# Kernel optimization log

Measured on AMD Instinct MI355X. Metric: run time of the kernel, lower is better.

Reference implementation:

```python
import jax, jax.numpy as jnp
import numpy as np
import math

def _ln(x, g, b, eps=1e-5):
    mu = x.mean(-1, keepdims=True)
    var = ((x - mu) ** 2).mean(-1, keepdims=True)
    return (x - mu) / jnp.sqrt(var + eps) * g + b

def _mha(x, in_w, in_b, out_w, out_b, nh):
    # torch nn.MultiheadAttention (batch_first, eval): q,k,v chunks of in_proj
    Bn, Nn, Dm = x.shape
    hd = Dm // nh
    q, k, v = jnp.split(x @ in_w.T + in_b, 3, axis=-1)
    sp = lambda t: t.reshape(Bn, Nn, nh, hd).transpose(0, 2, 1, 3)
    q, k, v = sp(q), sp(k), sp(v)
    a = jax.nn.softmax(jnp.einsum('bhid,bhjd->bhij', q, k) / math.sqrt(hd), axis=-1)
    y = jnp.einsum('bhij,bhjd->bhid', a, v).transpose(0, 2, 1, 3).reshape(Bn, Nn, Dm)
    return y @ out_w.T + out_b

def setup_inputs():
    key = jax.random.key(0)
    ks = iter(jax.random.split(key, 40))
    nrm = lambda shape: jax.random.normal(next(ks), shape, jnp.float32) * 0.02
    B, T, C, H, W = 2, 32, 3, 64, 64
    D, P, nL, nS = 512, 8, 6, 3
    N = (H // P) ** 2
    z = lambda *s: jnp.zeros(s, jnp.float32)
    o = lambda *s: jnp.ones(s, jnp.float32)
    return dict(
        x=jax.random.normal(next(ks), (B, T, C, H, W), jnp.float32),
        patch_w=nrm((D, C * P * P)), patch_b=z(D),
        tok_ln_g=o(D), tok_ln_b=z(D),
        spatial_pos=nrm((1, 1, N, D)), temporal_pos=nrm((1, T, 1, D)),
        snorm_g=o(D), snorm_b=z(D),
        sa_in_w=nrm((nS, 3 * D, D)), sa_in_b=z(nS, 3 * D),
        sa_out_w=nrm((nS, D, D)), sa_out_b=z(nS, D),
        ln1_g=o(nL, D), ln1_b=z(nL, D),
        kqv_w=nrm((nL, 3 * D, D)), kqv_b=z(nL, 3 * D),
        proj_w=nrm((nL, D, D)), proj_b=z(nL, D),
        ln2_g=o(nL, D), ln2_b=z(nL, D),
        fc_w=nrm((nL, 4 * D, D)), fc_b=z(nL, 4 * D),
        cproj_w=nrm((nL, D, 4 * D)), cproj_b=z(nL, D),
        lnf_g=o(D), lnf_b=z(D),
        th_w1=nrm((D // 2, D)), th_b1=z(D // 2), th_w2=nrm((1, D // 2)), th_b2=z(1),
        sh_w1=nrm((D // 2, D)), sh_b1=z(D // 2), sh_w2=nrm((1, D // 2)), sh_b2=z(1),
        pf_w1=nrm((D // 2, D)), pf_b1=z(D // 2), pf_w2=nrm((1, D // 2)), pf_b2=z(1),
    )

def reference(x, patch_w, patch_b, tok_ln_g, tok_ln_b, spatial_pos, temporal_pos,
              snorm_g, snorm_b, sa_in_w, sa_in_b, sa_out_w, sa_out_b,
              ln1_g, ln1_b, kqv_w, kqv_b, proj_w, proj_b, ln2_g, ln2_b,
              fc_w, fc_b, cproj_w, cproj_b, lnf_g, lnf_b,
              th_w1, th_b1, th_w2, th_b2, sh_w1, sh_b1, sh_w2, sh_b2,
              pf_w1, pf_b1, pf_w2, pf_b2):
    B, T, C, H, W = x.shape
    D = patch_w.shape[0]
    P = int(math.isqrt(patch_w.shape[1] // C))
    Hn, Wn = H // P, W // P
    N = Hn * Wn
    # Conv3d kernel=(1,P,P), stride=(1,P,P) == per-frame patchify + matmul
    patches = x.reshape(B, T, C, Hn, P, Wn, P).transpose(0, 1, 3, 5, 2, 4, 6).reshape(B, T, N, C * P * P)
    tok = _ln(patches @ patch_w.T + patch_b, tok_ln_g, tok_ln_b)
    tok = tok + spatial_pos + temporal_pos[:, :T]
    # per-frame spatial attention: identical math per frame -> batch over B*T
    s = tok.reshape(B * T, N, D)
    for i in range(sa_in_w.shape[0]):
        s = s + _mha(_ln(s, snorm_g, snorm_b), sa_in_w[i], sa_in_b[i], sa_out_w[i], sa_out_b[i], nh=4)
    L = T * N
    hid = s.reshape(B, L, D)
    nh = 8
    hd = D // nh
    mask = jnp.tril(jnp.ones((L, L), bool))  # causal over T*N tokens
    for i in range(kqv_w.shape[0]):
        a_in = _ln(hid, ln1_g[i], ln1_b[i])
        k, q, v = jnp.split(a_in @ kqv_w[i].T + kqv_b[i], 3, axis=-1)  # torch split order: k, q, v
        sp = lambda t: t.reshape(B, L, nh, hd).transpose(0, 2, 1, 3)
        q, k, v = sp(q), sp(k), sp(v)
        att = jnp.einsum('bhid,bhjd->bhij', q, k) / math.sqrt(hd)
        att = jax.nn.softmax(jnp.where(mask, att, -jnp.inf), axis=-1)
        y = jnp.einsum('bhij,bhjd->bhid', att, v).transpose(0, 2, 1, 3).reshape(B, L, D)
        hid = hid + y @ proj_w[i].T + proj_b[i]
        m_in = _ln(hid, ln2_g[i], ln2_b[i])
        h = jax.nn.gelu(m_in @ fc_w[i].T + fc_b[i], approximate=False)
        hid = hid + h @ cproj_w[i].T + cproj_b[i]
    hid = _ln(hid, lnf_g, lnf_b).reshape(B, T, N, D)
    head = lambda zz, w1, b1, w2, b2: jax.nn.leaky_relu(zz @ w1.T + b1, 0.2) @ w2.T + b2
    tf = hid.mean(axis=2)  # [B, T, D]
    temporal_score = head(tf[:, -1], th_w1, th_b1, th_w2, th_b2)  # [B, 1] (last timestep, full lengths)
    spatial_score = head(hid.mean(axis=1).mean(axis=1), sh_w1, sh_b1, sh_w2, sh_b2)
    per_frame_scores = head(tf, pf_w1, pf_b1, pf_w2, pf_b2)  # [B, T, 1]
    final_score = temporal_score + spatial_score + per_frame_scores.mean(axis=1)
    return (temporal_score, spatial_score, per_frame_scores, final_score)
```

## Files before the change

kernel.cpp:

```cpp
#include <hip/hip_runtime.h>
#include <hip/hip_bf16.h>
#include <math.h>

#define MTOK 4096

typedef __bf16 bf16x8 __attribute__((ext_vector_type(8)));
typedef float f32x4 __attribute__((ext_vector_type(4)));

__device__ __forceinline__ ushort f2bf(float f){
  __hip_bfloat16 h = __float2bfloat16(f);
  return *reinterpret_cast<ushort*>(&h);
}
__device__ __forceinline__ float bf2f(ushort u){
  return __uint_as_float(((uint)u) << 16);
}
__device__ __forceinline__ void gload_lds16(const void* g, void* l){
  __builtin_amdgcn_global_load_lds((__attribute__((address_space(1))) void*)(void*)g,
                                   (__attribute__((address_space(3))) void*)l, 16, 0, 0);
}

__device__ __forceinline__ float blockReduceSum(float v, float* red){
  #pragma unroll
  for (int off = 32; off; off >>= 1) v += __shfl_down(v, off, 64);
  int lane = threadIdx.x & 63, wid = threadIdx.x >> 6;
  __syncthreads();
  if (lane == 0) red[wid] = v;
  __syncthreads();
  float r = 0.f;
  int nw = blockDim.x >> 6;
  for (int i = 0; i < nw; i++) r += red[i];
  return r;
}
__device__ __forceinline__ float rowMax16(float v){
  #pragma unroll
  for (int m = 8; m; m >>= 1) v = fmaxf(v, __shfl_xor(v, m, 64));
  return v;
}
__device__ __forceinline__ float rowSum16(float v){
  #pragma unroll
  for (int m = 8; m; m >>= 1) v += __shfl_xor(v, m, 64);
  return v;
}

__global__ __launch_bounds__(256) void cvt_w_kernel(
    const float* __restrict__ src, ushort* __restrict__ dst, int n)
{
  int i = (blockIdx.x * 256 + threadIdx.x) * 8;
  float4 a = *(const float4*)(src + i);
  float4 b = *(const float4*)(src + i + 4);
  uint4 o;
  o.x = (uint)f2bf(a.x) | ((uint)f2bf(a.y) << 16);
  o.y = (uint)f2bf(a.z) | ((uint)f2bf(a.w) << 16);
  o.z = (uint)f2bf(b.x) | ((uint)f2bf(b.y) << 16);
  o.w = (uint)f2bf(b.z) | ((uint)f2bf(b.w) << 16);
  *(uint4*)(dst + i) = o;
}

#define OFF_PATCH 0u
#define OFF_SAIN  98304u
#define OFF_SAOUT 2457600u
#define OFF_KQV   3244032u
#define OFF_PROJ  7962624u
#define OFF_FC    9535488u
#define OFF_CPROJ 15826944u
#define W_TOTAL   22118400u
__global__ __launch_bounds__(256) void cvt_all_kernel(
    const float* __restrict__ pw, const float* __restrict__ sain,
    const float* __restrict__ saout, const float* __restrict__ kqv,
    const float* __restrict__ proj, const float* __restrict__ fc,
    const float* __restrict__ cproj, ushort* __restrict__ dst)
{
  int blk = blockIdx.x;
  const float* src; size_t off;
  if      (blk <    48){ src = pw;    off = OFF_PATCH; }
  else if (blk <  1200){ src = sain;  off = OFF_SAIN;  blk -= 48;   }
  else if (blk <  1584){ src = saout; off = OFF_SAOUT; blk -= 1200; }
  else if (blk <  3888){ src = kqv;   off = OFF_KQV;   blk -= 1584; }
  else if (blk <  4656){ src = proj;  off = OFF_PROJ;  blk -= 3888; }
  else if (blk <  7728){ src = fc;    off = OFF_FC;    blk -= 4656; }
  else                 { src = cproj; off = OFF_CPROJ; blk -= 7728; }
  size_t si = (size_t)blk*2048 + threadIdx.x*8;
  float4 a = *(const float4*)(src + si);
  float4 b = *(const float4*)(src + si + 4);
  uint4 o;
  o.x = (uint)f2bf(a.x) | ((uint)f2bf(a.y) << 16);
  o.y = (uint)f2bf(a.z) | ((uint)f2bf(a.w) << 16);
  o.z = (uint)f2bf(b.x) | ((uint)f2bf(b.y) << 16);
  o.w = (uint)f2bf(b.z) | ((uint)f2bf(b.w) << 16);
  *(uint4*)(dst + off + si) = o;
}

__global__ __launch_bounds__(256) void im2col_kernel(
    const float* __restrict__ x, ushort* __restrict__ Pm)
{
  int idx = blockIdx.x*256 + threadIdx.x;
  int m = idx / 24, e8 = idx % 24;
  int b = m >> 11, t = (m >> 6) & 31, n = m & 63;
  int hn = n >> 3, wn = n & 7;
  int c = e8 >> 3, ph = e8 & 7;
  const float* src = x + (((size_t)(b*32 + t)*3 + c)*64 + hn*8 + ph)*64 + wn*8;
  float4 a = *(const float4*)src;
  float4 bq = *(const float4*)(src + 4);
  uint4 o;
  o.x = (uint)f2bf(a.x) | ((uint)f2bf(a.y) << 16);
  o.y = (uint)f2bf(a.z) | ((uint)f2bf(a.w) << 16);
  o.z = (uint)f2bf(bq.x) | ((uint)f2bf(bq.y) << 16);
  o.w = (uint)f2bf(bq.z) | ((uint)f2bf(bq.w) << 16);
  *(uint4*)(Pm + (size_t)m*192 + e8*8) = o;
}

__global__ __launch_bounds__(256) void ln_pos_kernel(
    const float* __restrict__ in, float* __restrict__ out,
    const float* __restrict__ g, const float* __restrict__ b,
    const float* __restrict__ spos, const float* __restrict__ tpos)
{
  int r = blockIdx.x*4 + (threadIdx.x >> 6);
  int lane = threadIdx.x & 63;
  int n = r & 63, t = (r >> 6) & 31;
  const float* row = in + (size_t)r*512 + lane*8;
  float4 v0 = *(const float4*)row;
  float4 v1 = *(const float4*)(row + 4);
  float s = v0.x+v0.y+v0.z+v0.w+v1.x+v1.y+v1.z+v1.w;
  float q = v0.x*v0.x+v0.y*v0.y+v0.z*v0.z+v0.w*v0.w+v1.x*v1.x+v1.y*v1.y+v1.z*v1.z+v1.w*v1.w;
  #pragma unroll
  for (int m = 1; m < 64; m <<= 1){ s += __shfl_xor(s, m, 64); q += __shfl_xor(q, m, 64); }
  float mu = s*(1.f/512.f);
  float inv = rsqrtf(q*(1.f/512.f) - mu*mu + 1e-5f);
  const float* gp = g + lane*8;
  const float* bp = b + lane*8;
  const float* sp = spos + n*512 + lane*8;
  const float* tp = tpos + t*512 + lane*8;
  float* op = out + (size_t)r*512 + lane*8;
  #pragma unroll
  for (int e = 0; e < 2; e++){
    float4 vv = e ? v1 : v0;
    float4 gg = *(const float4*)(gp + e*4);
    float4 bb = *(const float4*)(bp + e*4);
    float4 ss = *(const float4*)(sp + e*4);
    float4 tt = *(const float4*)(tp + e*4);
    float4 oo;
    oo.x = (vv.x-mu)*inv*gg.x + bb.x + ss.x + tt.x;
    oo.y = (vv.y-mu)*inv*gg.y + bb.y + ss.y + tt.y;
    oo.z = (vv.z-mu)*inv*gg.z + bb.z + ss.z + tt.z;
    oo.w = (vv.w-mu)*inv*gg.w + bb.w + ss.w + tt.w;
    *(float4*)(op + e*4) = oo;
  }
}

__global__ __launch_bounds__(256) void ln_bf16_kernel(
    const float* __restrict__ in, ushort* __restrict__ out,
    const float* __restrict__ g, const float* __restrict__ b)
{
  int r = blockIdx.x*4 + (threadIdx.x >> 6);
  int lane = threadIdx.x & 63;
  const float* row = in + (size_t)r*512 + lane*8;
  float4 v0 = *(const float4*)row;
  float4 v1 = *(const float4*)(row + 4);
  float s = v0.x+v0.y+v0.z+v0.w+v1.x+v1.y+v1.z+v1.w;
  float q = v0.x*v0.x+v0.y*v0.y+v0.z*v0.z+v0.w*v0.w+v1.x*v1.x+v1.y*v1.y+v1.z*v1.z+v1.w*v1.w;
  #pragma unroll
  for (int m = 1; m < 64; m <<= 1){ s += __shfl_xor(s, m, 64); q += __shfl_xor(q, m, 64); }
  float mu = s*(1.f/512.f);
  float inv = rsqrtf(q*(1.f/512.f) - mu*mu + 1e-5f);
  float4 g0 = *(const float4*)(g + lane*8);
  float4 g1 = *(const float4*)(g + lane*8 + 4);
  float4 b0 = *(const float4*)(b + lane*8);
  float4 b1 = *(const float4*)(b + lane*8 + 4);
  uint4 o;
  o.x = (uint)f2bf((v0.x-mu)*inv*g0.x + b0.x) | ((uint)f2bf((v0.y-mu)*inv*g0.y + b0.y) << 16);
  o.y = (uint)f2bf((v0.z-mu)*inv*g0.z + b0.z) | ((uint)f2bf((v0.w-mu)*inv*g0.w + b0.w) << 16);
  o.z = (uint)f2bf((v1.x-mu)*inv*g1.x + b1.x) | ((uint)f2bf((v1.y-mu)*inv*g1.y + b1.y) << 16);
  o.w = (uint)f2bf((v1.z-mu)*inv*g1.z + b1.z) | ((uint)f2bf((v1.w-mu)*inv*g1.w + b1.w) << 16);
  *(uint4*)(out + (size_t)r*512 + lane*8) = o;
}

template<int BM, int BN, bool GELU, bool BF16OUT>
__global__ __launch_bounds__(256) void gemm2_kernel(
    const ushort* __restrict__ X, const ushort* __restrict__ Wb,
    const float* __restrict__ bias, const float* __restrict__ res,
    void* __restrict__ Yv, int M, int Nn, int K)
{
  constexpr int WROWS = (BN == 128) ? 2 : 4;
  constexpr int WM = BM / WROWS;
  constexpr int FM = WM / 16;
  constexpr int FN = 4;
  __shared__ __attribute__((aligned(16))) char smem[2*(BM+BN)*128];
  char* Xs0 = smem;
  char* Ws0 = smem + BM*128;
  char* Xs1 = smem + (BM+BN)*128;
  char* Ws1 = Xs1 + BM*128;
  int tid = threadIdx.x, lane = tid & 63, wv = tid >> 6;
  int bm = blockIdx.y * BM, bn = blockIdx.x * BN;
  int wm, wn;
  if (BN == 128){ wm = (wv >> 1) * WM; wn = (wv & 1) * 64; }
  else          { wm = wv * WM;        wn = 0; }

  f32x4 acc[FM][FN];
  #pragma unroll
  for (int i = 0; i < FM; i++)
    #pragma unroll
    for (int j = 0; j < FN; j++){ f32x4 z = {0.f,0.f,0.f,0.f}; acc[i][j] = z; }

  int rowoff = wv*8 + (lane >> 3);
  int colsrc = ((lane & 7) ^ (lane >> 3)) * 16;

  auto stage = [&](char* Xd, char* Wd, int k0){
    #pragma unroll
    for (int i = 0; i < BM/32; i++){
      int row = i*32 + rowoff;
      gload_lds16((const char*)(X + (size_t)(bm + row)*K + k0) + colsrc,
                  Xd + (i*32 + wv*8)*128);
    }
    #pragma unroll
    for (int i = 0; i < BN/32; i++){
      int row = i*32 + rowoff;
      gload_lds16((const char*)(Wb + (size_t)(bn + row)*K + k0) + colsrc,
                  Wd + (i*32 + wv*8)*128);
    }
  };

  stage(Xs0, Ws0, 0);
  __syncthreads();
  int nt = K >> 6;
  for (int t = 0; t < nt; t++){
    char* Xc = (t & 1) ? Xs1 : Xs0;
    char* Wc = (t & 1) ? Ws1 : Ws0;
    if (t + 1 < nt) stage((t & 1) ? Xs0 : Xs1, (t & 1) ? Ws0 : Ws1, (t+1)*64);
    #pragma unroll
    for (int kc = 0; kc < 2; kc++){
      bf16x8 a[FM], b[FN];
      #pragma unroll
      for (int f = 0; f < FM; f++){
        int ra = wm + f*16 + (lane & 15);
        a[f] = *(const bf16x8*)(Xc + ra*128 + ((kc*64 + (lane>>4)*16) ^ ((ra & 7) << 4)));
      }
      #pragma unroll
      for (int f = 0; f < FN; f++){
        int rb = wn + f*16 + (lane & 15);
        b[f] = *(const bf16x8*)(Wc + rb*128 + ((kc*64 + (lane>>4)*16) ^ ((rb & 7) << 4)));
      }
      #pragma unroll
      for (int i = 0; i < FM; i++)
        #pragma unroll
        for (int j = 0; j < FN; j++)
          acc[i][j] = __builtin_amdgcn_mfma_f32_16x16x32_bf16(a[i], b[j], acc[i][j], 0, 0, 0);
    }
    __syncthreads();
  }
  int col0 = lane & 15;
  float bv[FN];
  #pragma unroll
  for (int fn = 0; fn < FN; fn++) bv[fn] = bias[bn + wn + fn*16 + col0];
  #pragma unroll
  for (int fm = 0; fm < FM; fm++){
    #pragma unroll
    for (int r = 0; r < 4; r++){
      int m = bm + wm + fm*16 + (lane >> 4)*4 + r;
      #pragma unroll
      for (int fn = 0; fn < FN; fn++){
        int n = bn + wn + fn*16 + col0;
        float v = acc[fm][fn][r] + bv[fn];
        if (res) v += res[(size_t)m*Nn + n];
        if (GELU) v = 0.5f * v * (1.f + erff(v * 0.70710678118654752440f));
        if (BF16OUT) ((ushort*)Yv)[(size_t)m*Nn + n] = f2bf(v);
        else         ((float*) Yv)[(size_t)m*Nn + n] = v;
      }
    }
  }
}

__global__ __launch_bounds__(256) void spatial_attn_mfma_kernel(
    const ushort* __restrict__ qkv, ushort* __restrict__ y)
{
  __shared__ __attribute__((aligned(16))) char Ks[64*256];
  __shared__ __attribute__((aligned(16))) char Vt[128*128];
  __shared__ __attribute__((aligned(16))) char Ps[64*128];
  int bt = blockIdx.x, h = blockIdx.y;
  int tid = threadIdx.x, lane = tid & 63, w = tid >> 6;
  const ushort* base = qkv + (size_t)bt*64*1536 + (size_t)h*128;
  const float scale = 0.08838834764831845f;

  int qrow = w*16 + (lane & 15);
  bf16x8 qa[4];
  #pragma unroll
  for (int kc = 0; kc < 4; kc++)
    qa[kc] = *(const bf16x8*)(base + (size_t)qrow*1536 + kc*32 + (lane>>4)*8);

  #pragma unroll
  for (int i = 0; i < 4; i++){
    int row = w*16 + i*4 + (lane >> 4);
    const char* src = (const char*)(base + (size_t)row*1536 + 512) + (((lane & 15) ^ (row & 15)) * 16);
    char* dst = Ks + (w*16 + i*4)*256;
    gload_lds16(src, dst);
  }
  {
    int vj = (tid & 31) * 2;
    int d0 = (tid >> 5) * 16;
    const ushort* v0p = base + (size_t)vj*1536 + 1024 + d0;
    const ushort* v1p = v0p + 1536;
    uint4 a0 = *(const uint4*)(v0p);
    uint4 a1 = *(const uint4*)(v0p + 8);
    uint4 b0 = *(const uint4*)(v1p);
    uint4 b1 = *(const uint4*)(v1p + 8);
    uint av[8] = {a0.x, a0.y, a0.z, a0.w, a1.x, a1.y, a1.z, a1.w};
    uint bv[8] = {b0.x, b0.y, b0.z, b0.w, b1.x, b1.y, b1.z, b1.w};
    int cb = 4 * (tid & 31);
    #pragma unroll
    for (int e = 0; e < 8; e++){
      int dl = d0 + e*2, dh = dl + 1;
      uint vlo = (av[e] & 0xffffu) | ((bv[e] & 0xffffu) << 16);
      uint vhi = (av[e] >> 16) | (bv[e] & 0xffff0000u);
      *(uint*)(Vt + dl*128 + (cb ^ ((dl & 7) << 4))) = vlo;
      *(uint*)(Vt + dh*128 + (cb ^ ((dh & 7) << 4))) = vhi;
    }
  }
  __syncthreads();

  f32x4 zero4 = {0.f,0.f,0.f,0.f};
  f32x4 accS[4];
  __builtin_amdgcn_s_setprio(1);
  #pragma unroll
  for (int jt = 0; jt < 4; jt++){
    accS[jt] = zero4;
    #pragma unroll
    for (int kc = 0; kc < 4; kc++){
      int krow = jt*16 + (lane & 15);
      bf16x8 kb = *(const bf16x8*)(Ks + krow*256 + ((kc*64 + (lane>>4)*16) ^ ((krow & 15) << 4)));
      accS[jt] = __builtin_amdgcn_mfma_f32_16x16x32_bf16(qa[kc], kb, accS[jt], 0, 0, 0);
    }
  }
  __builtin_amdgcn_s_setprio(0);
  float l_sum[4];
  #pragma unroll
  for (int r = 0; r < 4; r++){
    float mx = fmaxf(fmaxf(accS[0][r], accS[1][r]), fmaxf(accS[2][r], accS[3][r]));
    mx = rowMax16(mx);
    int prow = w*16 + (lane>>4)*4 + r;
    int swz = (prow & 7) << 4;
    char* pbase = Ps + prow*128;
    float ps = 0.f;
    #pragma unroll
    for (int jt = 0; jt < 4; jt++){
      float p = __expf((accS[jt][r] - mx) * scale);
      ushort pb = f2bf(p);
      *(ushort*)(pbase + ((2*(jt*16 + (lane & 15))) ^ swz)) = pb;
      ps += bf2f(pb);
    }
    l_sum[r] = rowSum16(ps);
  }
  bf16x8 pa[2];
  #pragma unroll
  for (int kc2 = 0; kc2 < 2; kc2++){
    int prow = w*16 + (lane & 15);
    pa[kc2] = *(const bf16x8*)(Ps + prow*128 + ((kc2*64 + (lane>>4)*16) ^ ((prow & 7) << 4)));
  }
  f32x4 o[8];
  __builtin_amdgcn_s_setprio(1);
  #pragma unroll
  for (int dt = 0; dt < 8; dt++){
    o[dt] = zero4;
    #pragma unroll
    for (int kc2 = 0; kc2 < 2; kc2++){
      int vrow = dt*16 + (lane & 15);
      bf16x8 vb = *(const bf16x8*)(Vt + vrow*128 + ((kc2*64 + (lane>>4)*16) ^ ((vrow & 7) << 4)));
      o[dt] = __builtin_amdgcn_mfma_f32_16x16x32_bf16(pa[kc2], vb, o[dt], 0, 0, 0);
    }
  }
  __builtin_amdgcn_s_setprio(0);
  #pragma unroll
  for (int r = 0; r < 4; r++){
    float invl = 1.f / l_sum[r];
    int token = bt*64 + w*16 + (lane>>4)*4 + r;
    ushort* yrow = y + (size_t)token*512 + h*128;
    #pragma unroll
    for (int dt = 0; dt < 8; dt++)
      yrow[dt*16 + (lane & 15)] = f2bf(o[dt][r] * invl);
  }
}

__global__ __launch_bounds__(256) void temporal_attn_split_kernel(
    const ushort* __restrict__ qkv, ushort* __restrict__ Op, float* __restrict__ ml)
{
  __shared__ __attribute__((aligned(16))) char Ks[64*128];
  __shared__ __attribute__((aligned(16))) char Vt[64*128];
  __shared__ __attribute__((aligned(16))) char Ps[4*16*128];
  int id = blockIdx.x;
  int bh = id & 15;
  int rest = id >> 4;
  int qt = 31 - (rest >> 1);
  int half = rest & 1;
  int b = bh >> 3, h = bh & 7;
  int tid = threadIdx.x, lane = tid & 63, w = tid >> 6;
  int g = lane >> 4, q = lane & 15;
  const ushort* base = qkv + (size_t)(b*2048)*1536 + h*64;

  int nk = qt + 1;
  int ktm = (nk + 1) >> 1;
  int kt0 = half ? ktm : 0;
  int kt1 = half ? nk : ktm;

  int qrow = qt*64 + w*16 + q;
  bf16x8 qb[2];
  #pragma unroll
  for (int kc = 0; kc < 2; kc++)
    qb[kc] = *(const bf16x8*)(base + (size_t)qrow*1536 + 512 + kc*32 + g*8);

  f32x4 zero4 = {0.f,0.f,0.f,0.f};
  f32x4 o[4];
  #pragma unroll
  for (int dt = 0; dt < 4; dt++) o[dt] = zero4;
  float m_old = -1e30f, l_sum = 0.f;

  int kcolsrc = ((lane & 7) ^ (lane >> 3)) * 16;
  int vj  = (tid & 31) * 2;
  int vd0 = (tid >> 5) * 8;
  int vcb = 4 * (tid & 31);
  char* myP = Ps + w*2048;
  int pswz = (q & 7) << 4;

  for (int kt = kt0; kt < kt1; kt++){
    __syncthreads();
    #pragma unroll
    for (int i = 0; i < 2; i++){
      int row = w*16 + i*8 + (lane >> 3);
      gload_lds16((const char*)(base + (size_t)(kt*64 + row)*1536) + kcolsrc,
                  Ks + (w*16 + i*8)*128);
    }
    {
      const ushort* v0p = base + (size_t)(kt*64 + vj)*1536 + 1024 + vd0;
      const ushort* v1p = v0p + 1536;
      uint4 a0 = *(const uint4*)v0p;
      uint4 b0 = *(const uint4*)v1p;
      uint av[4] = {a0.x, a0.y, a0.z, a0.w};
      uint bv[4] = {b0.x, b0.y, b0.z, b0.w};
      #pragma unroll
      for (int e = 0; e < 4; e++){
        int dl = vd0 + e*2, dh = dl + 1;
        uint vlo = (av[e] & 0xffffu) | ((bv[e] & 0xffffu) << 16);
        uint vhi = (av[e] >> 16) | (bv[e] & 0xffff0000u);
        *(uint*)(Vt + dl*128 + (vcb ^ ((dl & 7) << 4))) = vlo;
        *(uint*)(Vt + dh*128 + (vcb ^ ((dh & 7) << 4))) = vhi;
      }
    }
    __syncthreads();

    f32x4 accS[4];
    __builtin_amdgcn_s_setprio(1);
    #pragma unroll
    for (int jt = 0; jt < 4; jt++){
      accS[jt] = zero4;
      #pragma unroll
      for (int kc = 0; kc < 2; kc++){
        int krow = jt*16 + q;
        bf16x8 kb = *(const bf16x8*)(Ks + krow*128 + ((kc*64 + g*16) ^ ((krow & 7) << 4)));
        accS[jt] = __builtin_amdgcn_mfma_f32_16x16x32_bf16(kb, qb[kc], accS[jt], 0, 0, 0);
      }
    }
    __builtin_amdgcn_s_setprio(0);
    if (kt == qt){
      int gi = qt*64 + w*16 + q;
      #pragma unroll
      for (int jt = 0; jt < 4; jt++)
        #pragma unroll
        for (int r = 0; r < 4; r++){
          int gj = kt*64 + jt*16 + g*4 + r;
          if (gj > gi) accS[jt][r] = -1e30f;
        }
    }
    float mloc = fmaxf(fmaxf(accS[0][0], accS[0][1]), fmaxf(accS[0][2], accS[0][3]));
    #pragma unroll
    for (int jt = 1; jt < 4; jt++){
      float t2 = fmaxf(fmaxf(accS[jt][0], accS[jt][1]), fmaxf(accS[jt][2], accS[jt][3]));
      mloc = fmaxf(mloc, t2);
    }
    mloc *= 0.125f;
    mloc = fmaxf(mloc, __shfl_xor(mloc, 16, 64));
    mloc = fmaxf(mloc, __shfl_xor(mloc, 32, 64));
    float mnew = fmaxf(m_old, mloc);
    float corr = __expf(m_old - mnew);
    float ps = 0.f;
    #pragma unroll
    for (int jt = 0; jt < 4; jt++){
      ushort pb0 = f2bf(__expf(accS[jt][0]*0.125f - mnew));
      ushort pb1 = f2bf(__expf(accS[jt][1]*0.125f - mnew));
      ushort pb2 = f2bf(__expf(accS[jt][2]*0.125f - mnew));
      ushort pb3 = f2bf(__expf(accS[jt][3]*0.125f - mnew));
      ps += bf2f(pb0) + bf2f(pb1) + bf2f(pb2) + bf2f(pb3);
      uint2 wv;
      wv.x = (uint)pb0 | ((uint)pb1 << 16);
      wv.y = (uint)pb2 | ((uint)pb3 << 16);
      *(uint2*)(myP + q*128 + ((jt*32 + g*8) ^ pswz)) = wv;
    }
    l_sum = l_sum*corr + ps;
    m_old = mnew;
    #pragma unroll
    for (int dt = 0; dt < 4; dt++) o[dt] *= corr;

    bf16x8 pfr[2];
    #pragma unroll
    for (int kc2 = 0; kc2 < 2; kc2++)
      pfr[kc2] = *(const bf16x8*)(myP + q*128 + ((kc2*64 + g*16) ^ pswz));
    __builtin_amdgcn_s_setprio(1);
    #pragma unroll
    for (int dt = 0; dt < 4; dt++){
      #pragma unroll
      for (int kc2 = 0; kc2 < 2; kc2++){
        int vrow = dt*16 + q;
        bf16x8 vb = *(const bf16x8*)(Vt + vrow*128 + ((kc2*64 + g*16) ^ ((vrow & 7) << 4)));
        o[dt] = __builtin_amdgcn_mfma_f32_16x16x32_bf16(vb, pfr[kc2], o[dt], 0, 0, 0);
      }
    }
    __builtin_amdgcn_s_setprio(0);
  }
  l_sum += __shfl_xor(l_sum, 16, 64);
  l_sum += __shfl_xor(l_sum, 32, 64);
  size_t tokbase = (size_t)half*4096 + (size_t)b*2048;
  int token = qt*64 + w*16 + q;
  ushort* yrow = Op + (tokbase + token)*512 + h*64;
  #pragma unroll
  for (int dt = 0; dt < 4; dt++){
    ushort4 o4;
    o4.x = f2bf(o[dt][0]); o4.y = f2bf(o[dt][1]);
    o4.z = f2bf(o[dt][2]); o4.w = f2bf(o[dt][3]);
    *(ushort4*)(yrow + dt*16 + g*4) = o4;
  }
  if (g == 0){
    float* mlp = ml + ((tokbase + token)*8 + h)*2;
    mlp[0] = m_old;
    mlp[1] = l_sum;
  }
}

__global__ __launch_bounds__(256) void attn_merge_kernel(
    const ushort* __restrict__ Op, const float* __restrict__ ml, ushort* __restrict__ Ef)
{
  int tok = blockIdx.x*4 + (threadIdx.x >> 6);
  int l6 = threadIdx.x & 63;
  int h = l6 >> 3, d0 = (l6 & 7)*8;
  int e = h*64 + d0;
  const float* m1p = ml + ((size_t)tok*8 + h)*2;
  const float* m2p = ml + (((size_t)4096 + tok)*8 + h)*2;
  float m1 = m1p[0], l1 = m1p[1];
  float m2 = m2p[0], l2 = m2p[1];
  float mm = fmaxf(m1, m2);
  float w1 = __expf(m1 - mm), w2 = __expf(m2 - mm);
  float inv = 1.f / (w1*l1 + w2*l2);
  uint4 a = *(const uint4*)(Op + (size_t)tok*512 + e);
  uint4 bq = *(const uint4*)(Op + ((size_t)4096 + tok)*512 + e);
  uint av[4] = {a.x, a.y, a.z, a.w};
  uint bv[4] = {bq.x, bq.y, bq.z, bq.w};
  uint ov[4];
  #pragma unroll
  for (int p = 0; p < 4; p++){
    float x0 = (w1*bf2f((ushort)(av[p] & 0xffff)) + w2*bf2f((ushort)(bv[p] & 0xffff))) * inv;
    float x1 = (w1*bf2f((ushort)(av[p] >> 16))    + w2*bf2f((ushort)(bv[p] >> 16)))    * inv;
    ov[p] = (uint)f2bf(x0) | ((uint)f2bf(x1) << 16);
  }
  uint4 o; o.x = ov[0]; o.y = ov[1]; o.z = ov[2]; o.w = ov[3];
  *(uint4*)(Ef + (size_t)tok*512 + e) = o;
}

__global__ __launch_bounds__(256) void reduce_tf_kernel(const ushort* __restrict__ hid, float* __restrict__ tf){
  int bt = blockIdx.x, tid = threadIdx.x;
  for (int d = tid; d < 512; d += 256){
    float s = 0.f;
    for (int n = 0; n < 64; n++) s += bf2f(hid[((size_t)bt*64 + n)*512 + d]);
    tf[(size_t)bt*512 + d] = s * (1.f/64.f);
  }
}

__global__ __launch_bounds__(256) void head_kernel(
    const float* __restrict__ tf,
    const float* __restrict__ th_w1, const float* __restrict__ th_b1,
    const float* __restrict__ th_w2, const float* __restrict__ th_b2,
    const float* __restrict__ sh_w1, const float* __restrict__ sh_b1,
    const float* __restrict__ sh_w2, const float* __restrict__ sh_b2,
    const float* __restrict__ pf_w1, const float* __restrict__ pf_b1,
    const float* __restrict__ pf_w2, const float* __restrict__ pf_b2,
    float* __restrict__ out)
{
  __shared__ float z[512];
  __shared__ float red[4];
  int bi = blockIdx.x, tid = threadIdx.x;
  const float *w1, *b1, *w2, *b2;
  float* dst;
  if (bi < 64){
    w1 = pf_w1; b1 = pf_b1; w2 = pf_w2; b2 = pf_b2; dst = out + 4 + bi;
    z[tid]       = tf[(size_t)bi*512 + tid];
    z[tid + 256] = tf[(size_t)bi*512 + tid + 256];
  } else if (bi < 66){
    int b = bi - 64;
    w1 = th_w1; b1 = th_b1; w2 = th_w2; b2 = th_b2; dst = out + b;
    z[tid]       = tf[(size_t)(b*32 + 31)*512 + tid];
    z[tid + 256] = tf[(size_t)(b*32 + 31)*512 + tid + 256];
  } else {
    int b = bi - 66;
    w1 = sh_w1; b1 = sh_b1; w2 = sh_w2; b2 = sh_b2; dst = out + 2 + b;
    float s0 = 0.f, s1 = 0.f;
    for (int t = 0; t < 32; t++){
      s0 += tf[(size_t)(b*32 + t)*512 + tid];
      s1 += tf[(size_t)(b*32 + t)*512 + tid + 256];
    }
    z[tid] = s0 * (1.f/32.f); z[tid + 256] = s1 * (1.f/32.f);
  }
  __syncthreads();
  float a = b1[tid];
  const float* wrow = w1 + (size_t)tid * 512;
  for (int k = 0; k < 512; k++) a = fmaf(wrow[k], z[k], a);
  a = (a > 0.f) ? a : 0.2f * a;
  float s = blockReduceSum(a * w2[tid], red);
  if (tid == 0) *dst = s + b2[0];
}

__global__ __launch_bounds__(64) void final_kernel(float* __restrict__ out){
  int b = threadIdx.x;
  if (b < 2){
    float s = 0.f;
    for (int t = 0; t < 32; t++) s += out[4 + b*32 + t];
    out[68 + b] = out[b] + out[2 + b] + s * (1.f/32.f);
  }
}

extern "C" void kernel_launch(void* const* d_in, const int* in_sizes, int n_in,
                              void* d_out, int out_size, void* d_ws, size_t ws_size,
                              hipStream_t stream)
{
  const float* x          = (const float*)d_in[0];
  const float* patch_w    = (const float*)d_in[1];
  const float* patch_b    = (const float*)d_in[2];
  const float* tok_ln_g   = (const float*)d_in[3];
  const float* tok_ln_b   = (const float*)d_in[4];
  const float* spatial_pos= (const float*)d_in[5];
  const float* temporal_pos=(const float*)d_in[6];
  const float* snorm_g    = (const float*)d_in[7];
  const float* snorm_b    = (const float*)d_in[8];
  const float* sa_in_w    = (const float*)d_in[9];
  const float* sa_in_b    = (const float*)d_in[10];
  const float* sa_out_w   = (const float*)d_in[11];
  const float* sa_out_b   = (const float*)d_in[12];
  const float* ln1_g      = (const float*)d_in[13];
  const float* ln1_b      = (const float*)d_in[14];
  const float* kqv_w      = (const float*)d_in[15];
  const float* kqv_b      = (const float*)d_in[16];
  const float* proj_w     = (const float*)d_in[17];
  const float* proj_b     = (const float*)d_in[18];
  const float* ln2_g      = (const float*)d_in[19];
  const float* ln2_b      = (const float*)d_in[20];
  const float* fc_w       = (const float*)d_in[21];
  const float* fc_b       = (const float*)d_in[22];
  const float* cproj_w    = (const float*)d_in[23];
  const float* cproj_b    = (const float*)d_in[24];
  const float* lnf_g      = (const float*)d_in[25];
  const float* lnf_b      = (const float*)d_in[26];
  const float* th_w1 = (const float*)d_in[27];
  const float* th_b1 = (const float*)d_in[28];
  const float* th_w2 = (const float*)d_in[29];
  const float* th_b2 = (const float*)d_in[30];
  const float* sh_w1 = (const float*)d_in[31];
  const float* sh_b1 = (const float*)d_in[32];
  const float* sh_w2 = (const float*)d_in[33];
  const float* sh_b2 = (const float*)d_in[34];
  const float* pf_w1 = (const float*)d_in[35];
  const float* pf_b1 = (const float*)d_in[36];
  const float* pf_w2 = (const float*)d_in[37];
  const float* pf_b2 = (const float*)d_in[38];

  float* out = (float*)d_out;
  char* p = (char*)d_ws;
  float*  A  = (float*)p;      p += (size_t)MTOK*512*4;
  ushort* Ru = (ushort*)p;     p += (size_t)MTOK*2048*2;
  ushort* Bf = (ushort*)p;     p += (size_t)MTOK*512*2;
  ushort* Ef = (ushort*)p;     p += (size_t)MTOK*512*2;
  float*  tfp = (float*)p;     p += (size_t)64*512*4;
  ushort* OpB = (ushort*)p;    p += (size_t)2*MTOK*512*2;
  float*  mlB = (float*)p;     p += (size_t)2*MTOK*8*2*4;
  ushort* Wslot = (ushort*)p;  p += (size_t)1048576*2;
  ushort* Wall = (ushort*)p;   p += (size_t)W_TOTAL*2;
  const size_t NEED_BIG = (size_t)(p - (char*)d_ws);
  float*  Pf = (float*)Ru;
  ushort* Pm = Ef;

  const bool big = (ws_size >= NEED_BIG);

  if (big){
    cvt_all_kernel<<<10800, 256, 0, stream>>>(patch_w, sa_in_w, sa_out_w, kqv_w,
                                              proj_w, fc_w, cproj_w, Wall);
  }
  auto W = [&](const float* src, size_t arena_off, size_t nelem) -> const ushort* {
    if (big) return Wall + arena_off;
    cvt_w_kernel<<<(int)(nelem/2048), 256, 0, stream>>>(src, Wslot, (int)nelem);
    return Wslot;
  };

  im2col_kernel<<<384, 256, 0, stream>>>(x, Pm);
  gemm2_kernel<64,64,false,false><<<dim3(8, 64), 256, 0, stream>>>(
      Pm, W(patch_w, OFF_PATCH, 512*192), patch_b, nullptr, Pf, MTOK, 512, 192);
  ln_pos_kernel<<<1024, 256, 0, stream>>>(Pf, A, tok_ln_g, tok_ln_b, spatial_pos, temporal_pos);

  for (int i = 0; i < 3; i++){
    ln_bf16_kernel<<<1024, 256, 0, stream>>>(A, Bf, snorm_g, snorm_b);
    gemm2_kernel<64,128,false,true><<<dim3(12, 64), 256, 0, stream>>>(
        Bf, W(sa_in_w + (size_t)i*1536*512, OFF_SAIN + (size_t)i*786432, 1536*512),
        sa_in_b + (size_t)i*1536, nullptr, Ru, MTOK, 1536, 512);
    spatial_attn_mfma_kernel<<<dim3(64, 4), 256, 0, stream>>>(Ru, Ef);
    gemm2_kernel<64,64,false,false><<<dim3(8, 64), 256, 0, stream>>>(
        Ef, W(sa_out_w + (size_t)i*512*512, OFF_SAOUT + (size_t)i*262144, 512*512),
        sa_out_b + (size_t)i*512, A, A, MTOK, 512, 512);
  }
  for (int i = 0; i < 6; i++){
    ln_bf16_kernel<<<1024, 256, 0, stream>>>(A, Bf, ln1_g + (size_t)i*512, ln1_b + (size_t)i*512);
    gemm2_kernel<64,128,false,true><<<dim3(12, 64), 256, 0, stream>>>(
        Bf, W(kqv_w + (size_t)i*1536*512, OFF_KQV + (size_t)i*786432, 1536*512),
        kqv_b + (size_t)i*1536, nullptr, Ru, MTOK, 1536, 512);
    temporal_attn_split_kernel<<<1024, 256, 0, stream>>>(Ru, OpB, mlB);
    attn_merge_kernel<<<1024, 256, 0, stream>>>(OpB, mlB, Ef);
    gemm2_kernel<64,64,false,false><<<dim3(8, 64), 256, 0, stream>>>(
        Ef, W(proj_w + (size_t)i*512*512, OFF_PROJ + (size_t)i*262144, 512*512),
        proj_b + (size_t)i*512, A, A, MTOK, 512, 512);
    ln_bf16_kernel<<<1024, 256, 0, stream>>>(A, Bf, ln2_g + (size_t)i*512, ln2_b + (size_t)i*512);
    gemm2_kernel<64,128,true,true><<<dim3(16, 64), 256, 0, stream>>>(
        Bf, W(fc_w + (size_t)i*2048*512, OFF_FC + (size_t)i*1048576, 2048*512),
        fc_b + (size_t)i*2048, nullptr, Ru, MTOK, 2048, 512);
    gemm2_kernel<64,64,false,false><<<dim3(8, 64), 256, 0, stream>>>(
        Ru, W(cproj_w + (size_t)i*512*2048, OFF_CPROJ + (size_t)i*1048576, 512*2048),
        cproj_b + (size_t)i*512, A, A, MTOK, 512, 2048);
  }
  ln_bf16_kernel<<<1024, 256, 0, stream>>>(A, Bf, lnf_g, lnf_b);
  reduce_tf_kernel<<<64, 256, 0, stream>>>(Bf, tfp);
  head_kernel<<<68, 256, 0, stream>>>(tfp, th_w1, th_b1, th_w2, th_b2,
                                      sh_w1, sh_b1, sh_w2, sh_b2,
                                      pf_w1, pf_b1, pf_w2, pf_b2, out);
  final_kernel<<<1, 64, 0, stream>>>(out);
}
```

Before: 806.2 us.

## Split-K cproj GEMM, shrink QKV/FC tiles, add lazy softmax rescale

```diff
diff --git a/kernel.cpp b/kernel.cpp
--- a/kernel.cpp
+++ b/kernel.cpp
@@ -178,7 +178,7 @@
 __global__ __launch_bounds__(256) void gemm2_kernel(
     const ushort* __restrict__ X, const ushort* __restrict__ Wb,
     const float* __restrict__ bias, const float* __restrict__ res,
-    void* __restrict__ Yv, int M, int Nn, int K)
+    void* __restrict__ Yv, int M, int Nn, int K, int kstride, int zko, size_t zyo)
 {
   constexpr int WROWS = (BN == 128) ? 2 : 4;
   constexpr int WM = BM / WROWS;
@@ -191,6 +191,10 @@
   char* Ws1 = Xs1 + BM*128;
   int tid = threadIdx.x, lane = tid & 63, wv = tid >> 6;
   int bm = blockIdx.y * BM, bn = blockIdx.x * BN;
+  int z = blockIdx.z;
+  X  += (size_t)z * zko;
+  Wb += (size_t)z * zko;
+  char* Yb = (char*)Yv + (size_t)z * zyo;
   int wm, wn;
   if (BN == 128){ wm = (wv >> 1) * WM; wn = (wv & 1) * 64; }
   else          { wm = wv * WM;        wn = 0; }
@@ -199,7 +203,7 @@
   #pragma unroll
   for (int i = 0; i < FM; i++)
     #pragma unroll
-    for (int j = 0; j < FN; j++){ f32x4 z = {0.f,0.f,0.f,0.f}; acc[i][j] = z; }
+    for (int j = 0; j < FN; j++){ f32x4 zz = {0.f,0.f,0.f,0.f}; acc[i][j] = zz; }
 
   int rowoff = wv*8 + (lane >> 3);
   int colsrc = ((lane & 7) ^ (lane >> 3)) * 16;
@@ -208,13 +212,13 @@
     #pragma unroll
     for (int i = 0; i < BM/32; i++){
       int row = i*32 + rowoff;
-      gload_lds16((const char*)(X + (size_t)(bm + row)*K + k0) + colsrc,
+      gload_lds16((const char*)(X + (size_t)(bm + row)*kstride + k0) + colsrc,
                   Xd + (i*32 + wv*8)*128);
     }
     #pragma unroll
     for (int i = 0; i < BN/32; i++){
       int row = i*32 + rowoff;
-      gload_lds16((const char*)(Wb + (size_t)(bn + row)*K + k0) + colsrc,
+      gload_lds16((const char*)(Wb + (size_t)(bn + row)*kstride + k0) + colsrc,
                   Wd + (i*32 + wv*8)*128);
     }
   };
@@ -250,7 +254,7 @@
   int col0 = lane & 15;
   float bv[FN];
   #pragma unroll
-  for (int fn = 0; fn < FN; fn++) bv[fn] = bias[bn + wn + fn*16 + col0];
+  for (int fn = 0; fn < FN; fn++) bv[fn] = bias ? bias[bn + wn + fn*16 + col0] : 0.f;
   #pragma unroll
   for (int fm = 0; fm < FM; fm++){
     #pragma unroll
@@ -262,11 +266,28 @@
         float v = acc[fm][fn][r] + bv[fn];
         if (res) v += res[(size_t)m*Nn + n];
         if (GELU) v = 0.5f * v * (1.f + erff(v * 0.70710678118654752440f));
-        if (BF16OUT) ((ushort*)Yv)[(size_t)m*Nn + n] = f2bf(v);
-        else         ((float*) Yv)[(size_t)m*Nn + n] = v;
+        if (BF16OUT) ((ushort*)Yb)[(size_t)m*Nn + n] = f2bf(v);
+        else         ((float*) Yb)[(size_t)m*Nn + n] = v;
       }
     }
   }
+}
+
+__global__ __launch_bounds__(256) void cproj_merge_kernel(
+    const float* __restrict__ Yp, const float* __restrict__ bias, float* __restrict__ A)
+{
+  int i = (blockIdx.x*256 + threadIdx.x) * 4;
+  int n = i & 511;
+  float4 y0 = *(const float4*)(Yp + i);
+  float4 y1 = *(const float4*)(Yp + (size_t)MTOK*512 + i);
+  float4 a  = *(const float4*)(A + i);
+  float4 b4 = *(const float4*)(bias + n);
+  float4 o;
+  o.x = a.x + b4.x + y0.x + y1.x;
+  o.y = a.y + b4.y + y0.y + y1.y;
+  o.z = a.z + b4.z + y0.z + y1.z;
+  o.w = a.w + b4.w + y0.w + y1.w;
+  *(float4*)(A + i) = o;
 }
 
 __global__ __launch_bounds__(256) void spatial_attn_mfma_kernel(
@@ -476,25 +497,28 @@
     mloc *= 0.125f;
     mloc = fmaxf(mloc, __shfl_xor(mloc, 16, 64));
     mloc = fmaxf(mloc, __shfl_xor(mloc, 32, 64));
-    float mnew = fmaxf(m_old, mloc);
-    float corr = __expf(m_old - mnew);
+    if (!__all(mloc <= m_old + 8.f)){
+      float mnew = fmaxf(m_old, mloc);
+      float corr = __expf(m_old - mnew);
+      l_sum *= corr;
+      #pragma unroll
+      for (int dt = 0; dt < 4; dt++) o[dt] *= corr;
+      m_old = mnew;
+    }
     float ps = 0.f;
     #pragma unroll
     for (int jt = 0; jt < 4; jt++){
-      ushort pb0 = f2bf(__expf(accS[jt][0]*0.125f - mnew));
-      ushort pb1 = f2bf(__expf(accS[jt][1]*0.125f - mnew));
-      ushort pb2 = f2bf(__expf(accS[jt][2]*0.125f - mnew));
-      ushort pb3 = f2bf(__expf(accS[jt][3]*0.125f - mnew));
+      ushort pb0 = f2bf(__expf(accS[jt][0]*0.125f - m_old));
+      ushort pb1 = f2bf(__expf(accS[jt][1]*0.125f - m_old));
+      ushort pb2 = f2bf(__expf(accS[jt][2]*0.125f - m_old));
+      ushort pb3 = f2bf(__expf(accS[jt][3]*0.125f - m_old));
       ps += bf2f(pb0) + bf2f(pb1) + bf2f(pb2) + bf2f(pb3);
       uint2 wv;
       wv.x = (uint)pb0 | ((uint)pb1 << 16);
       wv.y = (uint)pb2 | ((uint)pb3 << 16);
       *(uint2*)(myP + q*128 + ((jt*32 + g*8) ^ pswz)) = wv;
     }
-    l_sum = l_sum*corr + ps;
-    m_old = mnew;
-    #pragma unroll
-    for (int dt = 0; dt < 4; dt++) o[dt] *= corr;
+    l_sum += ps;
 
     bf16x8 pfr[2];
     #pragma unroll
@@ -677,10 +701,13 @@
   ushort* Wslot = (ushort*)p;  p += (size_t)1048576*2;
   ushort* Wall = (ushort*)p;   p += (size_t)W_TOTAL*2;
   const size_t NEED_BIG = (size_t)(p - (char*)d_ws);
+  float*  Yp = (float*)p;      p += (size_t)2*MTOK*512*4;
+  const size_t NEED_SPLIT = (size_t)(p - (char*)d_ws);
   float*  Pf = (float*)Ru;
   ushort* Pm = Ef;
 
-  const bool big = (ws_size >= NEED_BIG);
+  const bool big   = (ws_size >= NEED_BIG);
+  const bool ksplt = (ws_size >= NEED_SPLIT);
 
   if (big){
     cvt_all_kernel<<<10800, 256, 0, stream>>>(patch_w, sa_in_w, sa_out_w, kqv_w,
@@ -694,36 +721,42 @@
 
   im2col_kernel<<<384, 256, 0, stream>>>(x, Pm);
   gemm2_kernel<64,64,false,false><<<dim3(8, 64), 256, 0, stream>>>(
-      Pm, W(patch_w, OFF_PATCH, 512*192), patch_b, nullptr, Pf, MTOK, 512, 192);
+      Pm, W(patch_w, OFF_PATCH, 512*192), patch_b, nullptr, Pf, MTOK, 512, 192, 192, 0, 0);
   ln_pos_kernel<<<1024, 256, 0, stream>>>(Pf, A, tok_ln_g, tok_ln_b, spatial_pos, temporal_pos);
 
   for (int i = 0; i < 3; i++){
     ln_bf16_kernel<<<1024, 256, 0, stream>>>(A, Bf, snorm_g, snorm_b);
-    gemm2_kernel<64,128,false,true><<<dim3(12, 64), 256, 0, stream>>>(
+    gemm2_kernel<64,64,false,true><<<dim3(24, 64), 256, 0, stream>>>(
         Bf, W(sa_in_w + (size_t)i*1536*512, OFF_SAIN + (size_t)i*786432, 1536*512),
-        sa_in_b + (size_t)i*1536, nullptr, Ru, MTOK, 1536, 512);
+        sa_in_b + (size_t)i*1536, nullptr, Ru, MTOK, 1536, 512, 512, 0, 0);
     spatial_attn_mfma_kernel<<<dim3(64, 4), 256, 0, stream>>>(Ru, Ef);
     gemm2_kernel<64,64,false,false><<<dim3(8, 64), 256, 0, stream>>>(
         Ef, W(sa_out_w + (size_t)i*512*512, OFF_SAOUT + (size_t)i*262144, 512*512),
-        sa_out_b + (size_t)i*512, A, A, MTOK, 512, 512);
+        sa_out_b + (size_t)i*512, A, A, MTOK, 512, 512, 512, 0, 0);
   }
   for (int i = 0; i < 6; i++){
     ln_bf16_kernel<<<1024, 256, 0, stream>>>(A, Bf, ln1_g + (size_t)i*512, ln1_b + (size_t)i*512);
-    gemm2_kernel<64,128,false,true><<<dim3(12, 64), 256, 0, stream>>>(
+    gemm2_kernel<64,64,false,true><<<dim3(24, 64), 256, 0, stream>>>(
         Bf, W(kqv_w + (size_t)i*1536*512, OFF_KQV + (size_t)i*786432, 1536*512),
-        kqv_b + (size_t)i*1536, nullptr, Ru, MTOK, 1536, 512);
+        kqv_b + (size_t)i*1536, nullptr, Ru, MTOK, 1536, 512, 512, 0, 0);
     temporal_attn_split_kernel<<<1024, 256, 0, stream>>>(Ru, OpB, mlB);
     attn_merge_kernel<<<1024, 256, 0, stream>>>(OpB, mlB, Ef);
     gemm2_kernel<64,64,false,false><<<dim3(8, 64), 256, 0, stream>>>(
         Ef, W(proj_w + (size_t)i*512*512, OFF_PROJ + (size_t)i*262144, 512*512),
-        proj_b + (size_t)i*512, A, A, MTOK, 512, 512);
+        proj_b + (size_t)i*512, A, A, MTOK, 512, 512, 512, 0, 0);
     ln_bf16_kernel<<<1024, 256, 0, stream>>>(A, Bf, ln2_g + (size_t)i*512, ln2_b + (size_t)i*512);
-    gemm2_kernel<64,128,true,true><<<dim3(16, 64), 256, 0, stream>>>(
+    gemm2_kernel<64,64,true,true><<<dim3(32, 64), 256, 0, stream>>>(
         Bf, W(fc_w + (size_t)i*2048*512, OFF_FC + (size_t)i*1048576, 2048*512),
-        fc_b + (size_t)i*2048, nullptr, Ru, MTOK, 2048, 512);
-    gemm2_kernel<64,64,false,false><<<dim3(8, 64), 256, 0, stream>>>(
-        Ru, W(cproj_w + (size_t)i*512*2048, OFF_CPROJ + (size_t)i*1048576, 512*2048),
-        cproj_b + (size_t)i*512, A, A, MTOK, 512, 2048);
+        fc_b + (size_t)i*2048, nullptr, Ru, MTOK, 2048, 512, 512, 0, 0);
+    const ushort* cw = W(cproj_w + (size_t)i*512*2048, OFF_CPROJ + (size_t)i*1048576, 512*2048);
+    if (ksplt){
+      gemm2_kernel<64,64,false,false><<<dim3(8, 64, 2), 256, 0, stream>>>(
+          Ru, cw, nullptr, nullptr, Yp, MTOK, 512, 1024, 2048, 1024, (size_t)MTOK*512*4);
+      cproj_merge_kernel<<<2048, 256, 0, stream>>>(Yp, cproj_b + (size_t)i*512, A);
+    } else {
+      gemm2_kernel<64,64,false,false><<<dim3(8, 64), 256, 0, stream>>>(
+          Ru, cw, cproj_b + (size_t)i*512, A, A, MTOK, 512, 2048, 2048, 0, 0);
+    }
   }
   ln_bf16_kernel<<<1024, 256, 0, stream>>>(A, Bf, lnf_g, lnf_b);
   reduce_tf_kernel<<<64, 256, 0, stream>>>(Bf, tfp);
```

New measurement: 853.2 us. 5.8% more time.
